# Kernel tuning notes

Measured on AMD Instinct MI355X. Metric: run time of the kernel, lower is better.

## Reference

```python
import jax, jax.numpy as jnp
import numpy as np

SMOOTH = 9.0   # self.labmda
EPS = 1e-8
MASK_VAL = -1.0

I, R, D = 64, 36, 1024   # n_image, n_regions, d
C, W = 64, 32            # n_caption, max_n_word


def setup_inputs() -> dict:
    key = jax.random.key(0)
    k1, k2, k3, k4 = jax.random.split(key, 4)
    imgs = jax.random.normal(k1, (I, R, D), dtype=jnp.float32)
    caps = jax.random.normal(k2, (C, W, D), dtype=jnp.float32)
    img_lens = jax.random.randint(k3, (I,), 1, R + 1)
    cap_lens = jnp.maximum(jax.random.randint(k4, (C,), 0, W + 1), 4)
    return {"imgs": imgs, "caps": caps, "img_lens": img_lens, "cap_lens": cap_lens}


def reference(imgs, caps, img_lens, cap_lens):
    # imgs: (I,R,D) images/regions; caps: (C,W,D); cap_lens: (C,)
    # Vectorized over captions: padded word positions are masked so the
    # per-caption word-dim l2norm matches the ragged torch loop exactly.
    wmask = jnp.arange(W)[None, :] < cap_lens[:, None]          # (C,W)
    wmask_f = wmask.astype(imgs.dtype)

    # attn[c,i,w,r] = <caps[c,w], imgs[i,r]>  (torch: bmm(context, queryT))
    attn = jnp.einsum('ird,cwd->ciwr', imgs, caps)              # (C,I,W,R)
    attn = jax.nn.leaky_relu(attn, 0.1)
    attn = attn * wmask_f[:, None, :, None]                     # zero padded words
    # l2norm over word dim (torch l2norm(attn, 2) on (I,R,W)): eps after sqrt
    norm_w = jnp.sqrt(jnp.sum(attn * attn, axis=2, keepdims=True)) + EPS
    attn = attn / norm_w
    # temperature-scaled softmax over regions
    attn = jax.nn.softmax(attn * SMOOTH, axis=3)                # (C,I,W,R)

    # weighted context per word, l2-normalized over feature dim
    wctx = jnp.einsum('ciwr,ird->ciwd', attn, imgs)             # (C,I,W,D)
    wctx = wctx / (jnp.sqrt(jnp.sum(wctx * wctx, axis=-1, keepdims=True)) + EPS)

    # cosine similarity between the word and its attended context
    cap_e = caps[:, None, :, :]                                 # (C,1,W,D)
    w12 = jnp.sum(cap_e * wctx, axis=-1)                        # (C,I,W)
    w1 = jnp.sqrt(jnp.sum(cap_e * cap_e, axis=-1))
    w2 = jnp.sqrt(jnp.sum(wctx * wctx, axis=-1))
    sim = w12 / jnp.maximum(w1 * w2, EPS)                       # (C,I,W)

    sim = jnp.where(wmask[:, None, :], sim, MASK_VAL)
    return jnp.transpose(sim, (1, 0, 2))                        # (I,C,W)
```

## Files before the change

### kernel.cpp

```cpp
#include <hip/hip_runtime.h>
#include <hip/hip_bf16.h>

#define IDIM 64
#define RDIM 36
#define DDIM 1024
#define CDIM 64
#define WDIM 32
#define SMOOTH 9.0f
#define EPSF 1e-8f

typedef __bf16 bf16_t;
typedef __bf16 bf16x8 __attribute__((ext_vector_type(8)));
typedef float f32x4 __attribute__((ext_vector_type(4)));

#define MFMA16(a, b, c) __builtin_amdgcn_mfma_f32_16x16x32_bf16((a), (b), (c), 0, 0, 0)

#define IMGSB_OFF 0
#define IMGSB_BYTES (IDIM * 4 * 8 * 3 * 512 * 2)
#define CAPSA_OFF (IMGSB_OFF + IMGSB_BYTES)
#define CAPSA_BYTES (CDIM * 4 * 8 * 2 * 512 * 2)
#define GF_OFF    (CAPSA_OFF + CAPSA_BYTES)
#define GF_BYTES  (IDIM * 384 * 8 * 2)
#define CAPN_OFF  (GF_OFF + GF_BYTES)

__global__ __launch_bounds__(256) void prep_kernel(
    const float* __restrict__ imgs, const float* __restrict__ caps,
    bf16_t* __restrict__ imgsB, bf16_t* __restrict__ capsA,
    float* __restrict__ capnorm) {
  int wv = threadIdx.x >> 6, ln = threadIdx.x & 63;
  int unit = blockIdx.x * 4 + wv;
  if (unit < IDIM * RDIM) {
    int i = unit / RDIM, r = unit % RDIM;
    int nt = r >> 4, l15 = r & 15;
    const float* src = imgs + (size_t)unit * DDIM;
#pragma unroll
    for (int itr = 0; itr < 2; ++itr) {
      int ch = itr * 64 + ln;
      int k = ch * 8;
      int wvk = ch >> 5, kk = (ch >> 2) & 7, qd = ch & 3;
      float4 v0 = *(const float4*)(src + k);
      float4 v1 = *(const float4*)(src + k + 4);
      bf16x8 p;
      p[0] = (bf16_t)v0.x; p[1] = (bf16_t)v0.y; p[2] = (bf16_t)v0.z; p[3] = (bf16_t)v0.w;
      p[4] = (bf16_t)v1.x; p[5] = (bf16_t)v1.y; p[6] = (bf16_t)v1.z; p[7] = (bf16_t)v1.w;
      size_t dst = ((((size_t)(i * 4 + wvk) * 8 + kk) * 3 + nt) * 64 + qd * 16 + l15) * 8;
      *(bf16x8*)(imgsB + dst) = p;
    }
  } else if (unit < IDIM * RDIM + CDIM * WDIM) {
    int rr = unit - IDIM * RDIM;
    int mt = (rr & 31) >> 4, l15 = rr & 15;
    int c = rr >> 5;
    const float* src = caps + (size_t)rr * DDIM;
    float ss = 0.f;
#pragma unroll
    for (int itr = 0; itr < 2; ++itr) {
      int ch = itr * 64 + ln;
      int k = ch * 8;
      int wvk = ch >> 5, kk = (ch >> 2) & 7, qd = ch & 3;
      float4 v0 = *(const float4*)(src + k);
      float4 v1 = *(const float4*)(src + k + 4);
      ss += v0.x * v0.x + v0.y * v0.y + v0.z * v0.z + v0.w * v0.w;
      ss += v1.x * v1.x + v1.y * v1.y + v1.z * v1.z + v1.w * v1.w;
      bf16x8 p;
      p[0] = (bf16_t)v0.x; p[1] = (bf16_t)v0.y; p[2] = (bf16_t)v0.z; p[3] = (bf16_t)v0.w;
      p[4] = (bf16_t)v1.x; p[5] = (bf16_t)v1.y; p[6] = (bf16_t)v1.z; p[7] = (bf16_t)v1.w;
      size_t dst = ((((size_t)(c * 4 + wvk) * 8 + kk) * 2 + mt) * 64 + qd * 16 + l15) * 8;
      *(bf16x8*)(capsA + dst) = p;
    }
#pragma unroll
    for (int off = 32; off >= 1; off >>= 1) ss += __shfl_xor(ss, off, 64);
    if (ln == 0) capnorm[rr] = sqrtf(ss);
  } else {
    int z = unit - (IDIM * RDIM + CDIM * WDIM);
    int i = z >> 5, wvk = (z >> 3) & 3, kk = z & 7;
    if ((ln & 15) >= 4) {
      bf16x8 zz;
#pragma unroll
      for (int q = 0; q < 8; ++q) zz[q] = (bf16_t)0.0f;
      size_t dst = ((((size_t)(i * 4 + wvk) * 8 + kk) * 3 + 2) * 64 + ln) * 8;
      *(bf16x8*)(imgsB + dst) = zz;
    }
  }
}

__global__ __launch_bounds__(256) void gram_kernel(
    const bf16_t* __restrict__ imgsB, bf16_t* __restrict__ Gfrag) {
  __shared__ float part[4][48][49];
  int i = blockIdx.x;
  int tid = threadIdx.x, wv = tid >> 6, ln = tid & 63;
  int l15 = ln & 15, qd = ln >> 4;
  const bf16_t* base = imgsB + (size_t)(i * 4 + wv) * 8 * 3 * 512;

  f32x4 acc[3][3];
#pragma unroll
  for (int mt = 0; mt < 3; ++mt)
#pragma unroll
    for (int nt = 0; nt < 3; ++nt) {
      f32x4 zf = {0.f, 0.f, 0.f, 0.f};
      acc[mt][nt] = zf;
    }
#pragma unroll
  for (int kk = 0; kk < 8; ++kk) {
    bf16x8 a[3];
#pragma unroll
    for (int nt = 0; nt < 3; ++nt)
      a[nt] = *(const bf16x8*)(base + ((size_t)(kk * 3 + nt) * 64 + ln) * 8);
#pragma unroll
    for (int mt = 0; mt < 3; ++mt)
#pragma unroll
      for (int nt = 0; nt < 3; ++nt)
        acc[mt][nt] = MFMA16(a[mt], a[nt], acc[mt][nt]);
  }
#pragma unroll
  for (int mt = 0; mt < 3; ++mt)
#pragma unroll
    for (int nt = 0; nt < 3; ++nt)
#pragma unroll
      for (int rg = 0; rg < 4; ++rg)
        part[wv][mt * 16 + qd * 4 + rg][nt * 16 + l15] = acc[mt][nt][rg];
  __syncthreads();
  for (int idx = tid; idx < 384; idx += 256) {
    int kk = idx / 192;
    int rem = idx - kk * 192;
    int nt = rem >> 6, lnn = rem & 63;
    int qd2 = lnn >> 4, l152 = lnn & 15;
    int n = nt * 16 + l152;
    bf16x8 pk;
#pragma unroll
    for (int j = 0; j < 8; ++j) {
      int k = kk * 32 + qd2 * 8 + j;
      float v = (k < 48) ? (part[0][k][n] + part[1][k][n] + part[2][k][n] + part[3][k][n]) : 0.f;
      pk[j] = (bf16_t)v;
    }
    *(bf16x8*)(Gfrag + ((size_t)i * 384 + idx) * 8) = pk;
  }
}

__global__ __launch_bounds__(256, 3) void main_kernel(
    const bf16_t* __restrict__ capsA, const bf16_t* __restrict__ imgsB,
    const bf16_t* __restrict__ Gfrag, const float* __restrict__ capnorm,
    const int* __restrict__ cap_lens, float* __restrict__ out) {
  __shared__ __align__(16) bf16_t attnS[4][32 * 72];

  int bx = blockIdx.x;
  int wv = threadIdx.x >> 6, ln = threadIdx.x & 63;
  int l15 = ln & 15, qd = ln >> 4;
  int xcd = bx & 7, t = bx >> 3;
  int c = t & 63, ih = t >> 6;
  int i = xcd * 8 + ih * 4 + wv;
  int clen = cap_lens[c];

  const bf16_t* Ab = capsA + (size_t)c * (4 * 8 * 2 * 512);
  const bf16_t* Bb = imgsB + (size_t)i * (4 * 8 * 3 * 512);

  f32x4 acc[2][3];
#pragma unroll
  for (int mt = 0; mt < 2; ++mt)
#pragma unroll
    for (int nt = 0; nt < 3; ++nt) {
      f32x4 zf = {0.f, 0.f, 0.f, 0.f};
      acc[mt][nt] = zf;
    }
#pragma unroll 4
  for (int s = 0; s < 32; ++s) {
    const bf16_t* ap = Ab + (size_t)s * 1024 + ln * 8;
    const bf16_t* bp = Bb + (size_t)s * 1536 + ln * 8;
    bf16x8 a0 = *(const bf16x8*)(ap);
    bf16x8 a1 = *(const bf16x8*)(ap + 512);
    bf16x8 b0 = *(const bf16x8*)(bp);
    bf16x8 b1 = *(const bf16x8*)(bp + 512);
    bf16x8 b2 = *(const bf16x8*)(bp + 1024);
    acc[0][0] = MFMA16(a0, b0, acc[0][0]);
    acc[0][1] = MFMA16(a0, b1, acc[0][1]);
    acc[0][2] = MFMA16(a0, b2, acc[0][2]);
    acc[1][0] = MFMA16(a1, b0, acc[1][0]);
    acc[1][1] = MFMA16(a1, b1, acc[1][1]);
    acc[1][2] = MFMA16(a1, b2, acc[1][2]);
  }

  const bf16_t* Gb = Gfrag + (size_t)i * 3072;
  bf16x8 ga[2][3];
#pragma unroll
  for (int kk = 0; kk < 2; ++kk)
#pragma unroll
    for (int nt = 0; nt < 3; ++nt)
      ga[kk][nt] = *(const bf16x8*)(Gb + ((size_t)(kk * 3 + nt) * 64 + ln) * 8);
  f32x4 cn0 = *(const f32x4*)(capnorm + c * 32 + qd * 4);
  f32x4 cn1 = *(const f32x4*)(capnorm + c * 32 + 16 + qd * 4);

  float attnv[2][3][4];
#pragma unroll
  for (int mt = 0; mt < 2; ++mt)
#pragma unroll
    for (int nt = 0; nt < 3; ++nt) {
      bool padn = (nt == 2) && (l15 >= 4);
#pragma unroll
      for (int rg = 0; rg < 4; ++rg) {
        float v = acc[mt][nt][rg];
        float l = (v > 0.f) ? v : 0.1f * v;
        int m = mt * 16 + qd * 4 + rg;
        if (m >= clen || padn) l = 0.f;
        attnv[mt][nt][rg] = l;
      }
    }

  float sinv[3];
#pragma unroll
  for (int nt = 0; nt < 3; ++nt) {
    float ns = 0.f;
#pragma unroll
    for (int mt = 0; mt < 2; ++mt)
#pragma unroll
      for (int rg = 0; rg < 4; ++rg) {
        float t2 = attnv[mt][nt][rg];
        ns += t2 * t2;
      }
    ns += __shfl_xor(ns, 16, 64);
    ns += __shfl_xor(ns, 32, 64);
    sinv[nt] = SMOOTH / (sqrtf(ns) + EPSF);
  }

  float Srow[2][4];
#pragma unroll
  for (int mt = 0; mt < 2; ++mt)
#pragma unroll
    for (int rg = 0; rg < 4; ++rg) {
      float z[3];
#pragma unroll
      for (int nt = 0; nt < 3; ++nt) {
        float v = attnv[mt][nt][rg] * sinv[nt];
        if (nt == 2 && l15 >= 4) v = -1e30f;
        z[nt] = v;
      }
      float mx = fmaxf(fmaxf(z[0], z[1]), z[2]);
#pragma unroll
      for (int off = 1; off < 16; off <<= 1) mx = fmaxf(mx, __shfl_xor(mx, off, 64));
      float e[3], es = 0.f;
#pragma unroll
      for (int nt = 0; nt < 3; ++nt) {
        e[nt] = __expf(z[nt] - mx);
        es += e[nt];
      }
#pragma unroll
      for (int off = 1; off < 16; off <<= 1) es += __shfl_xor(es, off, 64);
      float inv = 1.0f / es;
      float sac = 0.f;
#pragma unroll
      for (int nt = 0; nt < 3; ++nt) {
        float a = e[nt] * inv;
        attnv[mt][nt][rg] = a;
        sac += a * acc[mt][nt][rg];
      }
#pragma unroll
      for (int off = 1; off < 16; off <<= 1) sac += __shfl_xor(sac, off, 64);
      Srow[mt][rg] = sac;
    }

  bf16_t* as = &attnS[wv][0];
#pragma unroll
  for (int mt = 0; mt < 2; ++mt)
#pragma unroll
    for (int nt = 0; nt < 3; ++nt)
#pragma unroll
      for (int rg = 0; rg < 4; ++rg)
        as[(mt * 16 + qd * 4 + rg) * 72 + nt * 16 + l15] = (bf16_t)attnv[mt][nt][rg];
  {
    bf16x8 z8;
#pragma unroll
    for (int q = 0; q < 8; ++q) z8[q] = (bf16_t)0.0f;
    *(bf16x8*)(as + (ln >> 1) * 72 + 48 + (ln & 1) * 8) = z8;
  }
  bf16x8 fa[2][2];
#pragma unroll
  for (int mt = 0; mt < 2; ++mt)
#pragma unroll
    for (int kk = 0; kk < 2; ++kk)
      fa[mt][kk] = *(const bf16x8*)(as + (mt * 16 + l15) * 72 + kk * 32 + qd * 8);

  f32x4 y[2][3];
#pragma unroll
  for (int mt = 0; mt < 2; ++mt)
#pragma unroll
    for (int nt = 0; nt < 3; ++nt) {
      f32x4 zf = {0.f, 0.f, 0.f, 0.f};
      y[mt][nt] = zf;
    }
#pragma unroll
  for (int kk = 0; kk < 2; ++kk)
#pragma unroll
    for (int mt = 0; mt < 2; ++mt)
#pragma unroll
      for (int nt = 0; nt < 3; ++nt)
        y[mt][nt] = MFMA16(fa[mt][kk], ga[kk][nt], y[mt][nt]);

  float n2row[2][4];
#pragma unroll
  for (int mt = 0; mt < 2; ++mt)
#pragma unroll
    for (int rg = 0; rg < 4; ++rg) {
      float nn = 0.f;
#pragma unroll
      for (int nt = 0; nt < 3; ++nt) nn += y[mt][nt][rg] * attnv[mt][nt][rg];
#pragma unroll
      for (int off = 1; off < 16; off <<= 1) nn += __shfl_xor(nn, off, 64);
      n2row[mt][rg] = nn;
    }

  if (l15 < 2) {
    int mt = l15;
    f32x4 cn = mt ? cn1 : cn0;
    f32x4 o;
#pragma unroll
    for (int rg = 0; rg < 4; ++rg) {
      float n2v = fmaxf(n2row[mt][rg], 0.f);
      float nrm = sqrtf(n2v);
      float den = nrm + EPSF;
      float w12 = Srow[mt][rg] / den;
      float w2 = nrm / den;
      float sim = w12 / fmaxf(cn[rg] * w2, EPSF);
      int m = mt * 16 + qd * 4 + rg;
      if (m >= clen) sim = -1.0f;
      o[rg] = sim;
    }
    *(f32x4*)(out + ((size_t)i * CDIM + c) * WDIM + mt * 16 + qd * 4) = o;
  }
}

extern "C" void kernel_launch(void* const* d_in, const int* in_sizes, int n_in,
                              void* d_out, int out_size, void* d_ws, size_t ws_size,
                              hipStream_t stream) {
  const float* imgs = (const float*)d_in[0];
  const float* caps = (const float*)d_in[1];
  const int* cap_lens = (const int*)d_in[3];
  float* out = (float*)d_out;

  char* ws = (char*)d_ws;
  bf16_t* imgsB = (bf16_t*)(ws + IMGSB_OFF);
  bf16_t* capsA = (bf16_t*)(ws + CAPSA_OFF);
  bf16_t* Gfrag = (bf16_t*)(ws + GF_OFF);
  float* capnorm = (float*)(ws + CAPN_OFF);

  prep_kernel<<<1600, 256, 0, stream>>>(imgs, caps, imgsB, capsA, capnorm);
  gram_kernel<<<IDIM, 256, 0, stream>>>(imgsB, Gfrag);
  main_kernel<<<1024, 256, 0, stream>>>(capsA, imgsB, Gfrag, capnorm, cap_lens, out);
}
```

Before: 108.0 us.

## Process two captions per wave, restage prep through LDS, move capnorm to gram

```diff
diff --git a/kernel.cpp b/kernel.cpp
--- a/kernel.cpp
+++ b/kernel.cpp
@@ -11,6 +11,7 @@
 
 typedef __bf16 bf16_t;
 typedef __bf16 bf16x8 __attribute__((ext_vector_type(8)));
+typedef __bf16 bf16x4 __attribute__((ext_vector_type(4)));
 typedef float f32x4 __attribute__((ext_vector_type(4)));
 
 #define MFMA16(a, b, c) __builtin_amdgcn_mfma_f32_16x16x32_bf16((a), (b), (c), 0, 0, 0)
@@ -25,157 +26,195 @@
 
 __global__ __launch_bounds__(256) void prep_kernel(
     const float* __restrict__ imgs, const float* __restrict__ caps,
-    bf16_t* __restrict__ imgsB, bf16_t* __restrict__ capsA,
-    float* __restrict__ capnorm) {
-  int wv = threadIdx.x >> 6, ln = threadIdx.x & 63;
-  int unit = blockIdx.x * 4 + wv;
-  if (unit < IDIM * RDIM) {
-    int i = unit / RDIM, r = unit % RDIM;
-    int nt = r >> 4, l15 = r & 15;
-    const float* src = imgs + (size_t)unit * DDIM;
-#pragma unroll
-    for (int itr = 0; itr < 2; ++itr) {
-      int ch = itr * 64 + ln;
-      int k = ch * 8;
-      int wvk = ch >> 5, kk = (ch >> 2) & 7, qd = ch & 3;
-      float4 v0 = *(const float4*)(src + k);
-      float4 v1 = *(const float4*)(src + k + 4);
+    bf16_t* __restrict__ imgsB, bf16_t* __restrict__ capsA) {
+  __shared__ __align__(16) bf16_t ldsb[36 * 264];
+  int b = blockIdx.x, tid = threadIdx.x;
+  if (b < 256) {
+    int i = b >> 2, wvk = b & 3, ks = wvk * 256;
+    const float* src = imgs + (size_t)i * RDIM * DDIM + ks;
+#pragma unroll
+    for (int rep = 0; rep < 9; ++rep) {
+      int idx = rep * 256 + tid;
+      int row = idx >> 6, q = idx & 63;
+      float4 v = *(const float4*)(src + (size_t)row * DDIM + q * 4);
+      bf16x4 p;
+      p[0] = (bf16_t)v.x; p[1] = (bf16_t)v.y; p[2] = (bf16_t)v.z; p[3] = (bf16_t)v.w;
+      *(bf16x4*)&ldsb[row * 264 + q * 4] = p;
+    }
+    __syncthreads();
+    bf16_t* dst = imgsB + (size_t)(i * 4 + wvk) * 12288;
+#pragma unroll
+    for (int rep = 0; rep < 6; ++rep) {
+      int u = rep * 256 + tid;
+      int kk = u / 192, rem = u - kk * 192;
+      int nt = rem >> 6, lane = rem & 63, qd = lane >> 4, l15 = lane & 15;
+      int row = nt * 16 + l15;
       bf16x8 p;
-      p[0] = (bf16_t)v0.x; p[1] = (bf16_t)v0.y; p[2] = (bf16_t)v0.z; p[3] = (bf16_t)v0.w;
-      p[4] = (bf16_t)v1.x; p[5] = (bf16_t)v1.y; p[6] = (bf16_t)v1.z; p[7] = (bf16_t)v1.w;
-      size_t dst = ((((size_t)(i * 4 + wvk) * 8 + kk) * 3 + nt) * 64 + qd * 16 + l15) * 8;
-      *(bf16x8*)(imgsB + dst) = p;
-    }
-  } else if (unit < IDIM * RDIM + CDIM * WDIM) {
-    int rr = unit - IDIM * RDIM;
-    int mt = (rr & 31) >> 4, l15 = rr & 15;
-    int c = rr >> 5;
-    const float* src = caps + (size_t)rr * DDIM;
-    float ss = 0.f;
-#pragma unroll
-    for (int itr = 0; itr < 2; ++itr) {
-      int ch = itr * 64 + ln;
-      int k = ch * 8;
-      int wvk = ch >> 5, kk = (ch >> 2) & 7, qd = ch & 3;
-      float4 v0 = *(const float4*)(src + k);
-      float4 v1 = *(const float4*)(src + k + 4);
-      ss += v0.x * v0.x + v0.y * v0.y + v0.z * v0.z + v0.w * v0.w;
-      ss += v1.x * v1.x + v1.y * v1.y + v1.z * v1.z + v1.w * v1.w;
-      bf16x8 p;
-      p[0] = (bf16_t)v0.x; p[1] = (bf16_t)v0.y; p[2] = (bf16_t)v0.z; p[3] = (bf16_t)v0.w;
-      p[4] = (bf16_t)v1.x; p[5] = (bf16_t)v1.y; p[6] = (bf16_t)v1.z; p[7] = (bf16_t)v1.w;
-      size_t dst = ((((size_t)(c * 4 + wvk) * 8 + kk) * 2 + mt) * 64 + qd * 16 + l15) * 8;
-      *(bf16x8*)(capsA + dst) = p;
-    }
-#pragma unroll
-    for (int off = 32; off >= 1; off >>= 1) ss += __shfl_xor(ss, off, 64);
-    if (ln == 0) capnorm[rr] = sqrtf(ss);
+      if (row < 36) {
+        p = *(const bf16x8*)&ldsb[row * 264 + kk * 32 + qd * 8];
+      } else {
+#pragma unroll
+        for (int j = 0; j < 8; ++j) p[j] = (bf16_t)0.0f;
+      }
+      *(bf16x8*)(dst + (size_t)u * 8) = p;
+    }
   } else {
-    int z = unit - (IDIM * RDIM + CDIM * WDIM);
-    int i = z >> 5, wvk = (z >> 3) & 3, kk = z & 7;
-    if ((ln & 15) >= 4) {
-      bf16x8 zz;
-#pragma unroll
-      for (int q = 0; q < 8; ++q) zz[q] = (bf16_t)0.0f;
-      size_t dst = ((((size_t)(i * 4 + wvk) * 8 + kk) * 3 + 2) * 64 + ln) * 8;
-      *(bf16x8*)(imgsB + dst) = zz;
+    int bb = b - 256;
+    int c = bb >> 2, wvk = bb & 3, ks = wvk * 256;
+    const float* src = caps + (size_t)c * WDIM * DDIM + ks;
+#pragma unroll
+    for (int rep = 0; rep < 8; ++rep) {
+      int idx = rep * 256 + tid;
+      int row = idx >> 6, q = idx & 63;
+      float4 v = *(const float4*)(src + (size_t)row * DDIM + q * 4);
+      bf16x4 p;
+      p[0] = (bf16_t)v.x; p[1] = (bf16_t)v.y; p[2] = (bf16_t)v.z; p[3] = (bf16_t)v.w;
+      *(bf16x4*)&ldsb[row * 264 + q * 4] = p;
+    }
+    __syncthreads();
+    bf16_t* dst = capsA + (size_t)(c * 4 + wvk) * 8192;
+#pragma unroll
+    for (int rep = 0; rep < 4; ++rep) {
+      int u = rep * 256 + tid;
+      int kk = u >> 7, rem = u & 127;
+      int mt = rem >> 6, lane = rem & 63, qd = lane >> 4, l15 = lane & 15;
+      int row = mt * 16 + l15;
+      bf16x8 p = *(const bf16x8*)&ldsb[row * 264 + kk * 32 + qd * 8];
+      *(bf16x8*)(dst + (size_t)u * 8) = p;
     }
   }
 }
 
 __global__ __launch_bounds__(256) void gram_kernel(
-    const bf16_t* __restrict__ imgsB, bf16_t* __restrict__ Gfrag) {
+    const bf16_t* __restrict__ imgsB, const bf16_t* __restrict__ capsA,
+    bf16_t* __restrict__ Gfrag, float* __restrict__ capnorm) {
   __shared__ float part[4][48][49];
-  int i = blockIdx.x;
+  __shared__ float cnl[4][32];
+  int bx = blockIdx.x;
   int tid = threadIdx.x, wv = tid >> 6, ln = tid & 63;
   int l15 = ln & 15, qd = ln >> 4;
-  const bf16_t* base = imgsB + (size_t)(i * 4 + wv) * 8 * 3 * 512;
-
-  f32x4 acc[3][3];
-#pragma unroll
-  for (int mt = 0; mt < 3; ++mt)
-#pragma unroll
-    for (int nt = 0; nt < 3; ++nt) {
-      f32x4 zf = {0.f, 0.f, 0.f, 0.f};
-      acc[mt][nt] = zf;
-    }
-#pragma unroll
-  for (int kk = 0; kk < 8; ++kk) {
-    bf16x8 a[3];
-#pragma unroll
-    for (int nt = 0; nt < 3; ++nt)
-      a[nt] = *(const bf16x8*)(base + ((size_t)(kk * 3 + nt) * 64 + ln) * 8);
+  if (bx < 64) {
+    int i = bx;
+    const bf16_t* base = imgsB + (size_t)(i * 4 + wv) * 12288;
+    f32x4 acc[3][3];
 #pragma unroll
     for (int mt = 0; mt < 3; ++mt)
 #pragma unroll
+      for (int nt = 0; nt < 3; ++nt) {
+        f32x4 zf = {0.f, 0.f, 0.f, 0.f};
+        acc[mt][nt] = zf;
+      }
+#pragma unroll
+    for (int kk = 0; kk < 8; ++kk) {
+      bf16x8 a[3];
+#pragma unroll
       for (int nt = 0; nt < 3; ++nt)
-        acc[mt][nt] = MFMA16(a[mt], a[nt], acc[mt][nt]);
-  }
-#pragma unroll
-  for (int mt = 0; mt < 3; ++mt)
-#pragma unroll
-    for (int nt = 0; nt < 3; ++nt)
-#pragma unroll
-      for (int rg = 0; rg < 4; ++rg)
-        part[wv][mt * 16 + qd * 4 + rg][nt * 16 + l15] = acc[mt][nt][rg];
-  __syncthreads();
-  for (int idx = tid; idx < 384; idx += 256) {
-    int kk = idx / 192;
-    int rem = idx - kk * 192;
-    int nt = rem >> 6, lnn = rem & 63;
-    int qd2 = lnn >> 4, l152 = lnn & 15;
-    int n = nt * 16 + l152;
-    bf16x8 pk;
-#pragma unroll
-    for (int j = 0; j < 8; ++j) {
-      int k = kk * 32 + qd2 * 8 + j;
-      float v = (k < 48) ? (part[0][k][n] + part[1][k][n] + part[2][k][n] + part[3][k][n]) : 0.f;
-      pk[j] = (bf16_t)v;
-    }
-    *(bf16x8*)(Gfrag + ((size_t)i * 384 + idx) * 8) = pk;
+        a[nt] = *(const bf16x8*)(base + ((size_t)(kk * 3 + nt) * 64 + ln) * 8);
+#pragma unroll
+      for (int mt = 0; mt < 3; ++mt)
+#pragma unroll
+        for (int nt = 0; nt < 3; ++nt)
+          acc[mt][nt] = MFMA16(a[mt], a[nt], acc[mt][nt]);
+    }
+#pragma unroll
+    for (int mt = 0; mt < 3; ++mt)
+#pragma unroll
+      for (int nt = 0; nt < 3; ++nt)
+#pragma unroll
+        for (int rg = 0; rg < 4; ++rg)
+          part[wv][mt * 16 + qd * 4 + rg][nt * 16 + l15] = acc[mt][nt][rg];
+    __syncthreads();
+    for (int idx = tid; idx < 384; idx += 256) {
+      int kk = idx / 192;
+      int rem = idx - kk * 192;
+      int nt = rem >> 6, lnn = rem & 63;
+      int qd2 = lnn >> 4, l152 = lnn & 15;
+      int n = nt * 16 + l152;
+      bf16x8 pk;
+#pragma unroll
+      for (int j = 0; j < 8; ++j) {
+        int k = kk * 32 + qd2 * 8 + j;
+        float v = (k < 48) ? (part[0][k][n] + part[1][k][n] + part[2][k][n] + part[3][k][n]) : 0.f;
+        pk[j] = (bf16_t)v;
+      }
+      *(bf16x8*)(Gfrag + ((size_t)i * 384 + idx) * 8) = pk;
+    }
+  } else {
+    int c = bx - 64;
+    const bf16_t* base = capsA + (size_t)(c * 4 + wv) * 8192;
+    float ss0 = 0.f, ss1 = 0.f;
+#pragma unroll
+    for (int kk = 0; kk < 8; ++kk) {
+      bf16x8 p0 = *(const bf16x8*)(base + ((size_t)(kk * 2 + 0) * 64 + ln) * 8);
+      bf16x8 p1 = *(const bf16x8*)(base + ((size_t)(kk * 2 + 1) * 64 + ln) * 8);
+#pragma unroll
+      for (int j = 0; j < 8; ++j) {
+        float v0 = (float)p0[j], v1 = (float)p1[j];
+        ss0 += v0 * v0;
+        ss1 += v1 * v1;
+      }
+    }
+    ss0 += __shfl_xor(ss0, 16, 64); ss0 += __shfl_xor(ss0, 32, 64);
+    ss1 += __shfl_xor(ss1, 16, 64); ss1 += __shfl_xor(ss1, 32, 64);
+    if (qd == 0) { cnl[wv][l15] = ss0; cnl[wv][16 + l15] = ss1; }
+    __syncthreads();
+    if (tid < 32)
+      capnorm[c * 32 + tid] = sqrtf(cnl[0][tid] + cnl[1][tid] + cnl[2][tid] + cnl[3][tid]);
   }
 }
 
-__global__ __launch_bounds__(256, 3) void main_kernel(
+__global__ __launch_bounds__(256, 2) void main_kernel(
     const bf16_t* __restrict__ capsA, const bf16_t* __restrict__ imgsB,
     const bf16_t* __restrict__ Gfrag, const float* __restrict__ capnorm,
     const int* __restrict__ cap_lens, float* __restrict__ out) {
-  __shared__ __align__(16) bf16_t attnS[4][32 * 72];
+  __shared__ __align__(16) bf16_t attnS[8][2304];
 
   int bx = blockIdx.x;
   int wv = threadIdx.x >> 6, ln = threadIdx.x & 63;
   int l15 = ln & 15, qd = ln >> 4;
-  int xcd = bx & 7, t = bx >> 3;
-  int c = t & 63, ih = t >> 6;
-  int i = xcd * 8 + ih * 4 + wv;
-  int clen = cap_lens[c];
-
-  const bf16_t* Ab = capsA + (size_t)c * (4 * 8 * 2 * 512);
-  const bf16_t* Bb = imgsB + (size_t)i * (4 * 8 * 3 * 512);
-
-  f32x4 acc[2][3];
-#pragma unroll
-  for (int mt = 0; mt < 2; ++mt)
-#pragma unroll
-    for (int nt = 0; nt < 3; ++nt) {
-      f32x4 zf = {0.f, 0.f, 0.f, 0.f};
-      acc[mt][nt] = zf;
-    }
+  int xcd = bx & 7, rest = bx >> 3;
+  int ig = xcd * 2 + (rest & 1);
+  int cpair = rest >> 1;
+  int i = ig * 4 + wv;
+  int c0 = cpair * 2;
+  int clen[2] = {cap_lens[c0], cap_lens[c0 + 1]};
+
+  const bf16_t* Ab = capsA + (size_t)c0 * 32768;
+  const bf16_t* Bb = imgsB + (size_t)i * 49152;
+
+  f32x4 acc[2][2][3];
+#pragma unroll
+  for (int t = 0; t < 2; ++t)
+#pragma unroll
+    for (int mt = 0; mt < 2; ++mt)
+#pragma unroll
+      for (int nt = 0; nt < 3; ++nt) {
+        f32x4 zf = {0.f, 0.f, 0.f, 0.f};
+        acc[t][mt][nt] = zf;
+      }
 #pragma unroll 4
   for (int s = 0; s < 32; ++s) {
     const bf16_t* ap = Ab + (size_t)s * 1024 + ln * 8;
     const bf16_t* bp = Bb + (size_t)s * 1536 + ln * 8;
-    bf16x8 a0 = *(const bf16x8*)(ap);
-    bf16x8 a1 = *(const bf16x8*)(ap + 512);
+    bf16x8 a00 = *(const bf16x8*)(ap);
+    bf16x8 a01 = *(const bf16x8*)(ap + 512);
+    bf16x8 a10 = *(const bf16x8*)(ap + 32768);
+    bf16x8 a11 = *(const bf16x8*)(ap + 33280);
     bf16x8 b0 = *(const bf16x8*)(bp);
     bf16x8 b1 = *(const bf16x8*)(bp + 512);
     bf16x8 b2 = *(const bf16x8*)(bp + 1024);
-    acc[0][0] = MFMA16(a0, b0, acc[0][0]);
-    acc[0][1] = MFMA16(a0, b1, acc[0][1]);
-    acc[0][2] = MFMA16(a0, b2, acc[0][2]);
-    acc[1][0] = MFMA16(a1, b0, acc[1][0]);
-    acc[1][1] = MFMA16(a1, b1, acc[1][1]);
-    acc[1][2] = MFMA16(a1, b2, acc[1][2]);
+    acc[0][0][0] = MFMA16(a00, b0, acc[0][0][0]);
+    acc[0][0][1] = MFMA16(a00, b1, acc[0][0][1]);
+    acc[0][0][2] = MFMA16(a00, b2, acc[0][0][2]);
+    acc[0][1][0] = MFMA16(a01, b0, acc[0][1][0]);
+    acc[0][1][1] = MFMA16(a01, b1, acc[0][1][1]);
+    acc[0][1][2] = MFMA16(a01, b2, acc[0][1][2]);
+    acc[1][0][0] = MFMA16(a10, b0, acc[1][0][0]);
+    acc[1][0][1] = MFMA16(a10, b1, acc[1][0][1]);
+    acc[1][0][2] = MFMA16(a10, b2, acc[1][0][2]);
+    acc[1][1][0] = MFMA16(a11, b0, acc[1][1][0]);
+    acc[1][1][1] = MFMA16(a11, b1, acc[1][1][1]);
+    acc[1][1][2] = MFMA16(a11, b2, acc[1][1][2]);
   }
 
   const bf16_t* Gb = Gfrag + (size_t)i * 3072;
@@ -185,144 +224,145 @@
 #pragma unroll
     for (int nt = 0; nt < 3; ++nt)
       ga[kk][nt] = *(const bf16x8*)(Gb + ((size_t)(kk * 3 + nt) * 64 + ln) * 8);
-  f32x4 cn0 = *(const f32x4*)(capnorm + c * 32 + qd * 4);
-  f32x4 cn1 = *(const f32x4*)(capnorm + c * 32 + 16 + qd * 4);
-
-  float attnv[2][3][4];
-#pragma unroll
-  for (int mt = 0; mt < 2; ++mt)
+
+  float attnv[2][2][3][4];
+  float Srow[2][2][4];
+  float n2row[2][2][4];
+
+#pragma unroll
+  for (int t = 0; t < 2; ++t) {
+#pragma unroll
+    for (int mt = 0; mt < 2; ++mt)
+#pragma unroll
+      for (int nt = 0; nt < 3; ++nt) {
+        bool padn = (nt == 2) && (l15 >= 4);
+#pragma unroll
+        for (int rg = 0; rg < 4; ++rg) {
+          float v = acc[t][mt][nt][rg];
+          float l = (v > 0.f) ? v : 0.1f * v;
+          int m = mt * 16 + qd * 4 + rg;
+          if (m >= clen[t] || padn) l = 0.f;
+          attnv[t][mt][nt][rg] = l;
+        }
+      }
+    float sinv[3];
 #pragma unroll
     for (int nt = 0; nt < 3; ++nt) {
-      bool padn = (nt == 2) && (l15 >= 4);
+      float ns = 0.f;
+#pragma unroll
+      for (int mt = 0; mt < 2; ++mt)
+#pragma unroll
+        for (int rg = 0; rg < 4; ++rg) {
+          float t2 = attnv[t][mt][nt][rg];
+          ns += t2 * t2;
+        }
+      ns += __shfl_xor(ns, 16, 64);
+      ns += __shfl_xor(ns, 32, 64);
+      sinv[nt] = SMOOTH / (sqrtf(ns) + EPSF);
+    }
+#pragma unroll
+    for (int mt = 0; mt < 2; ++mt)
 #pragma unroll
       for (int rg = 0; rg < 4; ++rg) {
-        float v = acc[mt][nt][rg];
-        float l = (v > 0.f) ? v : 0.1f * v;
+        float z[3];
+#pragma unroll
+        for (int nt = 0; nt < 3; ++nt) {
+          float v = attnv[t][mt][nt][rg] * sinv[nt];
+          if (nt == 2 && l15 >= 4) v = -1e30f;
+          z[nt] = v;
+        }
+        float mx = fmaxf(fmaxf(z[0], z[1]), z[2]);
+#pragma unroll
+        for (int off = 1; off < 16; off <<= 1) mx = fmaxf(mx, __shfl_xor(mx, off, 64));
+        float e[3], es = 0.f;
+#pragma unroll
+        for (int nt = 0; nt < 3; ++nt) {
+          e[nt] = __expf(z[nt] - mx);
+          es += e[nt];
+        }
+#pragma unroll
+        for (int off = 1; off < 16; off <<= 1) es += __shfl_xor(es, off, 64);
+        float inv = 1.0f / es;
+        float sac = 0.f;
+#pragma unroll
+        for (int nt = 0; nt < 3; ++nt) {
+          float a = e[nt] * inv;
+          attnv[t][mt][nt][rg] = a;
+          sac += a * acc[t][mt][nt][rg];
+        }
+#pragma unroll
+        for (int off = 1; off < 16; off <<= 1) sac += __shfl_xor(sac, off, 64);
+        Srow[t][mt][rg] = sac;
+      }
+    bf16_t* as = &attnS[wv * 2 + t][0];
+#pragma unroll
+    for (int mt = 0; mt < 2; ++mt)
+#pragma unroll
+      for (int nt = 0; nt < 3; ++nt)
+#pragma unroll
+        for (int rg = 0; rg < 4; ++rg)
+          as[(mt * 16 + qd * 4 + rg) * 72 + nt * 16 + l15] = (bf16_t)attnv[t][mt][nt][rg];
+    {
+      bf16x8 z8;
+#pragma unroll
+      for (int q = 0; q < 8; ++q) z8[q] = (bf16_t)0.0f;
+      *(bf16x8*)(as + (ln >> 1) * 72 + 48 + (ln & 1) * 8) = z8;
+    }
+    bf16x8 fa[2][2];
+#pragma unroll
+    for (int mt = 0; mt < 2; ++mt)
+#pragma unroll
+      for (int kk = 0; kk < 2; ++kk)
+        fa[mt][kk] = *(const bf16x8*)(as + (mt * 16 + l15) * 72 + kk * 32 + qd * 8);
+    f32x4 y[2][3];
+#pragma unroll
+    for (int mt = 0; mt < 2; ++mt)
+#pragma unroll
+      for (int nt = 0; nt < 3; ++nt) {
+        f32x4 zf = {0.f, 0.f, 0.f, 0.f};
+        y[mt][nt] = zf;
+      }
+#pragma unroll
+    for (int kk = 0; kk < 2; ++kk)
+#pragma unroll
+      for (int mt = 0; mt < 2; ++mt)
+#pragma unroll
+        for (int nt = 0; nt < 3; ++nt)
+          y[mt][nt] = MFMA16(fa[mt][kk], ga[kk][nt], y[mt][nt]);
+#pragma unroll
+    for (int mt = 0; mt < 2; ++mt)
+#pragma unroll
+      for (int rg = 0; rg < 4; ++rg) {
+        float nn = 0.f;
+#pragma unroll
+        for (int nt = 0; nt < 3; ++nt) nn += y[mt][nt][rg] * attnv[t][mt][nt][rg];
+#pragma unroll
+        for (int off = 1; off < 16; off <<= 1) nn += __shfl_xor(nn, off, 64);
+        n2row[t][mt][rg] = nn;
+      }
+  }
+
+#pragma unroll
+  for (int t = 0; t < 2; ++t) {
+    if (l15 < 2) {
+      int mt = l15;
+      int c = c0 + t;
+      f32x4 cn = *(const f32x4*)(capnorm + c * 32 + mt * 16 + qd * 4);
+      f32x4 o;
+#pragma unroll
+      for (int rg = 0; rg < 4; ++rg) {
+        float n2v = fmaxf(n2row[t][mt][rg], 0.f);
+        float nrm = sqrtf(n2v);
+        float den = nrm + EPSF;
+        float w12 = Srow[t][mt][rg] / den;
+        float w2 = nrm / den;
+        float sim = w12 / fmaxf(cn[rg] * w2, EPSF);
         int m = mt * 16 + qd * 4 + rg;
-        if (m >= clen || padn) l = 0.f;
-        attnv[mt][nt][rg] = l;
-      }
-    }
-
-  float sinv[3];
-#pragma unroll
-  for (int nt = 0; nt < 3; ++nt) {
-    float ns = 0.f;
-#pragma unroll
-    for (int mt = 0; mt < 2; ++mt)
-#pragma unroll
-      for (int rg = 0; rg < 4; ++rg) {
-        float t2 = attnv[mt][nt][rg];
-        ns += t2 * t2;
-      }
-    ns += __shfl_xor(ns, 16, 64);
-    ns += __shfl_xor(ns, 32, 64);
-    sinv[nt] = SMOOTH / (sqrtf(ns) + EPSF);
-  }
-
-  float Srow[2][4];
-#pragma unroll
-  for (int mt = 0; mt < 2; ++mt)
-#pragma unroll
-    for (int rg = 0; rg < 4; ++rg) {
-      float z[3];
-#pragma unroll
-      for (int nt = 0; nt < 3; ++nt) {
-        float v = attnv[mt][nt][rg] * sinv[nt];
-        if (nt == 2 && l15 >= 4) v = -1e30f;
-        z[nt] = v;
-      }
-      float mx = fmaxf(fmaxf(z[0], z[1]), z[2]);
-#pragma unroll
-      for (int off = 1; off < 16; off <<= 1) mx = fmaxf(mx, __shfl_xor(mx, off, 64));
-      float e[3], es = 0.f;
-#pragma unroll
-      for (int nt = 0; nt < 3; ++nt) {
-        e[nt] = __expf(z[nt] - mx);
-        es += e[nt];
-      }
-#pragma unroll
-      for (int off = 1; off < 16; off <<= 1) es += __shfl_xor(es, off, 64);
-      float inv = 1.0f / es;
-      float sac = 0.f;
-#pragma unroll
-      for (int nt = 0; nt < 3; ++nt) {
-        float a = e[nt] * inv;
-        attnv[mt][nt][rg] = a;
-        sac += a * acc[mt][nt][rg];
-      }
-#pragma unroll
-      for (int off = 1; off < 16; off <<= 1) sac += __shfl_xor(sac, off, 64);
-      Srow[mt][rg] = sac;
-    }
-
-  bf16_t* as = &attnS[wv][0];
-#pragma unroll
-  for (int mt = 0; mt < 2; ++mt)
-#pragma unroll
-    for (int nt = 0; nt < 3; ++nt)
-#pragma unroll
-      for (int rg = 0; rg < 4; ++rg)
-        as[(mt * 16 + qd * 4 + rg) * 72 + nt * 16 + l15] = (bf16_t)attnv[mt][nt][rg];
-  {
-    bf16x8 z8;
-#pragma unroll
-    for (int q = 0; q < 8; ++q) z8[q] = (bf16_t)0.0f;
-    *(bf16x8*)(as + (ln >> 1) * 72 + 48 + (ln & 1) * 8) = z8;
-  }
-  bf16x8 fa[2][2];
-#pragma unroll
-  for (int mt = 0; mt < 2; ++mt)
-#pragma unroll
-    for (int kk = 0; kk < 2; ++kk)
-      fa[mt][kk] = *(const bf16x8*)(as + (mt * 16 + l15) * 72 + kk * 32 + qd * 8);
-
-  f32x4 y[2][3];
-#pragma unroll
-  for (int mt = 0; mt < 2; ++mt)
-#pragma unroll
-    for (int nt = 0; nt < 3; ++nt) {
-      f32x4 zf = {0.f, 0.f, 0.f, 0.f};
-      y[mt][nt] = zf;
-    }
-#pragma unroll
-  for (int kk = 0; kk < 2; ++kk)
-#pragma unroll
-    for (int mt = 0; mt < 2; ++mt)
-#pragma unroll
-      for (int nt = 0; nt < 3; ++nt)
-        y[mt][nt] = MFMA16(fa[mt][kk], ga[kk][nt], y[mt][nt]);
-
-  float n2row[2][4];
-#pragma unroll
-  for (int mt = 0; mt < 2; ++mt)
-#pragma unroll
-    for (int rg = 0; rg < 4; ++rg) {
-      float nn = 0.f;
-#pragma unroll
-      for (int nt = 0; nt < 3; ++nt) nn += y[mt][nt][rg] * attnv[mt][nt][rg];
-#pragma unroll
-      for (int off = 1; off < 16; off <<= 1) nn += __shfl_xor(nn, off, 64);
-      n2row[mt][rg] = nn;
-    }
-
-  if (l15 < 2) {
-    int mt = l15;
-    f32x4 cn = mt ? cn1 : cn0;
-    f32x4 o;
-#pragma unroll
-    for (int rg = 0; rg < 4; ++rg) {
-      float n2v = fmaxf(n2row[mt][rg], 0.f);
-      float nrm = sqrtf(n2v);
-      float den = nrm + EPSF;
-      float w12 = Srow[mt][rg] / den;
-      float w2 = nrm / den;
-      float sim = w12 / fmaxf(cn[rg] * w2, EPSF);
-      int m = mt * 16 + qd * 4 + rg;
-      if (m >= clen) sim = -1.0f;
-      o[rg] = sim;
-    }
-    *(f32x4*)(out + ((size_t)i * CDIM + c) * WDIM + mt * 16 + qd * 4) = o;
+        if (m >= clen[t]) sim = -1.0f;
+        o[rg] = sim;
+      }
+      *(f32x4*)(out + ((size_t)i * CDIM + c) * WDIM + mt * 16 + qd * 4) = o;
+    }
   }
 }
 
@@ -340,7 +380,7 @@
   bf16_t* Gfrag = (bf16_t*)(ws + GF_OFF);
   float* capnorm = (float*)(ws + CAPN_OFF);
 
-  prep_kernel<<<1600, 256, 0, stream>>>(imgs, caps, imgsB, capsA, capnorm);
-  gram_kernel<<<IDIM, 256, 0, stream>>>(imgsB, Gfrag);
-  main_kernel<<<1024, 256, 0, stream>>>(capsA, imgsB, Gfrag, capnorm, cap_lens, out);
+  prep_kernel<<<512, 256, 0, stream>>>(imgs, caps, imgsB, capsA);
+  gram_kernel<<<128, 256, 0, stream>>>(imgsB, capsA, Gfrag, capnorm);
+  main_kernel<<<512, 256, 0, stream>>>(capsA, imgsB, Gfrag, capnorm, cap_lens, out);
 }
```

New measurement: 117.5 us. +8.8%, slower.
